# Performance work log

Measured on AMD Instinct MI355X. Metric: run time of the kernel, lower is better.

The kernel has to match this reference:

```python
import jax, jax.numpy as jnp
import numpy as np


def setup_inputs() -> dict:
    key = jax.random.key(0)
    kq, kk, kv = jax.random.split(key, 3)
    B, L, S, H, E = 2, 2048, 2048, 8, 64
    queries = jax.random.normal(kq, (B, L, H, E), dtype=jnp.float32)
    keys = jax.random.normal(kk, (B, S, H, E), dtype=jnp.float32)
    values = jax.random.normal(kv, (B, S, H, E), dtype=jnp.float32)
    a1 = jnp.float32(1.0)
    a2 = jnp.float32(1.0)
    return {"queries": queries, "keys": keys, "values": values, "a1": a1, "a2": a2}


def reference(queries, keys, values, a1, a2):
    # queries: (B,L,H,E); keys/values: (B,S,H,E)
    E = queries.shape[-1]
    scale = 1.0 / jnp.sqrt(jnp.float32(E))
    # shared QK scores: (B,H,L,S)
    qk = jnp.einsum('blhe,bshe->bhls', queries, keys) * scale
    # sparse branch: relu^2 (dropout = identity in eval)
    ssa = jnp.square(jax.nn.relu(qk))
    ssa_out = jnp.einsum('bhls,bshd->blhd', ssa, values)
    # dense branch: softmax over keys
    dsa = jax.nn.softmax(qk, axis=-1)
    dsa_out = jnp.einsum('bhls,bshd->blhd', dsa, values)
    w1 = jnp.exp(a1)
    w2 = jnp.exp(a2)
    alpha1 = w1 / (w1 + w2)
    alpha2 = w2 / (w1 + w2)
    return alpha1 * ssa_out + alpha2 * dsa_out
```

## Files before the change

### kernel.cpp

```cpp
#include <hip/hip_runtime.h>

typedef short short4v __attribute__((ext_vector_type(4)));
typedef short short8v __attribute__((ext_vector_type(8)));
typedef float float4v __attribute__((ext_vector_type(4)));
typedef unsigned short u16;

#define NB 2
#define NL 2048
#define NS 2048
#define NH 8
#define NE 64
#define HE (NH*NE)
#define NLT (NL/64)
#define NST (NS/64)
#define TILE_U16 4096

static __device__ __forceinline__ unsigned pk2bf(float a, float b) {
  union { float f; unsigned u; } x, y; x.f = a; y.f = b;
  return __builtin_amdgcn_perm(y.u + 0x8000u, x.u + 0x8000u, 0x07060302u);
}

#define GLD16(gp, lp) __builtin_amdgcn_global_load_lds( \
    (const __attribute__((address_space(1))) void*)(gp), \
    (__attribute__((address_space(3))) void*)(lp), 16, 0, 0)

static __device__ __forceinline__ int fK(int s) { return (s & 3) | ((s >> 1) & 4); }

__global__ __launch_bounds__(256)
void prepack(const float* __restrict__ kp, const float* __restrict__ vp,
             u16* __restrict__ kimg, u16* __restrict__ vimg)
{
  __shared__ __align__(16) u16 ldsv[TILE_U16];

  const int bid  = blockIdx.x;
  const int tile = bid >> 1;
  const int doV  = bid & 1;
  const int st = tile & (NST - 1);
  const int bh = tile >> 5;
  const int h  = bh & (NH - 1);
  const int b  = bh >> 3;
  const int s0 = st * 64;
  const size_t base = (size_t)b * NS * HE + h * NE;
  const int tid  = threadIdx.x;
  const int wv   = tid >> 6;
  const int lane = tid & 63;
  const int ln7  = lane & 7;

  if (!doV) {
    u16* kt = kimg + (size_t)tile * TILE_U16;
    for (int slot = tid; slot < 512; slot += 256) {
      const int srow = slot >> 3, p = slot & 7, c = p ^ fK(srow);
      const float* src = kp + base + (size_t)(s0 + srow) * HE + c * 8;
      float4 x0 = *(const float4*)src;
      float4 x1 = *(const float4*)(src + 4);
      unsigned d[4] = { pk2bf(x0.x, x0.y), pk2bf(x0.z, x0.w),
                        pk2bf(x1.x, x1.y), pk2bf(x1.z, x1.w) };
      *(int4*)(kt + slot * 8) = *(const int4*)d;
    }
    return;
  }

  u16* vt = vimg + (size_t)tile * TILE_U16;
  {
    const float* vcol = vp + base + (size_t)(s0 + wv * 16) * HE + lane;
    unsigned vr[8];
    #pragma unroll
    for (int jj = 0; jj < 8; ++jj)
      vr[jj] = pk2bf(vcol[(size_t)(2 * jj) * HE], vcol[(size_t)(2 * jj + 1) * HE]);
    #pragma unroll
    for (int i = 0; i < 2; ++i) {
      const int cs = (2 * wv + i) ^ ln7;
      int4 t4 = make_int4((int)vr[4*i+0], (int)vr[4*i+1],
                          (int)vr[4*i+2], (int)vr[4*i+3]);
      *(int4*)(&ldsv[lane * 64 + cs * 8]) = t4;
    }
  }
  __syncthreads();
  {
    const int4* s = (const int4*)ldsv;
    int4* dst = (int4*)vt;
    dst[tid]       = s[tid];
    dst[tid + 256] = s[tid + 256];
  }
}

__global__ __launch_bounds__(256, 2)
void assa_fwd(const float* __restrict__ qp, const u16* __restrict__ kimg,
              const u16* __restrict__ vimg, const float* __restrict__ a1p,
              const float* __restrict__ a2p, float* __restrict__ op)
{
  __shared__ __align__(16) u16 ldsb[4][2 * TILE_U16];

  const int tid  = threadIdx.x;
  const int wv   = tid >> 6;
  const int lane = tid & 63;
  const int ln15 = lane & 15;
  const int ln7  = lane & 7;
  const int quad = lane >> 4;

  const int bid = blockIdx.x;
  const int bh  = bid & 15;
  const int lt  = bid >> 4;
  const int h   = bh & (NH - 1);
  const int b   = bh >> 3;

  const int lbase = lt * 64 + wv * 16;

  short8v qf0, qf1;
  {
    const float* qrow = qp + ((size_t)(b * NL + lbase + ln15)) * HE + h * NE + quad * 8;
    float4 q0 = *(const float4*)(qrow);
    float4 q1 = *(const float4*)(qrow + 4);
    float4 q2 = *(const float4*)(qrow + 32);
    float4 q3 = *(const float4*)(qrow + 36);
    unsigned d0[4] = { pk2bf(0.125f*q0.x, 0.125f*q0.y), pk2bf(0.125f*q0.z, 0.125f*q0.w),
                       pk2bf(0.125f*q1.x, 0.125f*q1.y), pk2bf(0.125f*q1.z, 0.125f*q1.w) };
    unsigned d1[4] = { pk2bf(0.125f*q2.x, 0.125f*q2.y), pk2bf(0.125f*q2.z, 0.125f*q2.w),
                       pk2bf(0.125f*q3.x, 0.125f*q3.y), pk2bf(0.125f*q3.z, 0.125f*q3.w) };
    qf0 = *(const short8v*)d0;
    qf1 = *(const short8v*)d1;
  }

  short8v ones8;
  #pragma unroll
  for (int j = 0; j < 8; ++j) ones8[j] = (short)0x3F80;

  const size_t tbase = (size_t)bh * NST;

  float4v acc_s[4], acc_d[4], acc_l;
  #pragma unroll
  for (int t = 0; t < 4; ++t)
    #pragma unroll
    for (int r = 0; r < 4; ++r) { acc_s[t][r] = 0.0f; acc_d[t][r] = 0.0f; }
  #pragma unroll
  for (int r = 0; r < 4; ++r) acc_l[r] = 0.0f;

  auto dma_tile = [&](int st, int nb) {
    const int hf = wv & 1;
    const u16* g;
    u16* l;
    if (wv < 2) {
      g = kimg + (tbase + st) * TILE_U16 + hf * 2048 + lane * 8;
      l = &ldsb[nb][hf * 2048];
    } else {
      g = vimg + (tbase + st) * TILE_U16 + hf * 2048 + lane * 8;
      l = &ldsb[nb][TILE_U16 + hf * 2048];
    }
    GLD16(g,        l);
    GLD16(g +  512, l +  512);
    GLD16(g + 1024, l + 1024);
    GLD16(g + 1536, l + 1536);
  };

  dma_tile(0, 0);
  dma_tile(1, 1);
  dma_tile(2, 2);

  const int rperm = 8 * (ln15 >> 2) + (ln15 & 3);
  const int fk    = (ln15 & 3) | (((ln15 >> 2) & 1) << 2);

  for (int st = 0; st < NST; ++st) {
    if (st + 2 < NST)      asm volatile("s_waitcnt vmcnt(8)" ::: "memory");
    else if (st + 1 < NST) asm volatile("s_waitcnt vmcnt(4)" ::: "memory");
    else                   asm volatile("s_waitcnt vmcnt(0)" ::: "memory");
    __builtin_amdgcn_s_barrier();
    asm volatile("" ::: "memory");
    if (st + 3 < NST) dma_tile(st + 3, (st + 3) & 3);

    const u16* kb_l = ldsb[st & 3];
    const u16* vb_l = ldsb[st & 3] + TILE_U16;

    #pragma unroll
    for (int U = 0; U < 2; ++U) {
      float4v sa0, sa1;
      #pragma unroll
      for (int r = 0; r < 4; ++r) { sa0[r] = 0.0f; sa1[r] = 0.0f; }
      const u16* krow0 = &kb_l[(32 * U + rperm) * 64];
      const u16* krow1 = krow0 + 4 * 64;
      short8v kf00 = *(const short8v*)(krow0 + (quad ^ fk) * 8);
      short8v kf01 = *(const short8v*)(krow0 + ((4 + quad) ^ fk) * 8);
      short8v kf10 = *(const short8v*)(krow1 + (quad ^ fk) * 8);
      short8v kf11 = *(const short8v*)(krow1 + ((4 + quad) ^ fk) * 8);
      __builtin_amdgcn_s_setprio(1);
      sa0 = __builtin_amdgcn_mfma_f32_16x16x32_bf16(kf00, qf0, sa0, 0, 0, 0);
      sa0 = __builtin_amdgcn_mfma_f32_16x16x32_bf16(kf01, qf1, sa0, 0, 0, 0);
      sa1 = __builtin_amdgcn_mfma_f32_16x16x32_bf16(kf10, qf0, sa1, 0, 0, 0);
      sa1 = __builtin_amdgcn_mfma_f32_16x16x32_bf16(kf11, qf1, sa1, 0, 0, 0);
      __builtin_amdgcn_s_setprio(0);

      float ps[8], pd[8];
      #pragma unroll
      for (int r = 0; r < 4; ++r) {
        float s0 = sa0[r], s1 = sa1[r];
        float r0 = s0 > 0.0f ? s0 : 0.0f;
        float r1 = s1 > 0.0f ? s1 : 0.0f;
        ps[r] = r0 * r0;  ps[4 + r] = r1 * r1;
        pd[r] = __expf(s0); pd[4 + r] = __expf(s1);
      }
      unsigned da[4] = { pk2bf(ps[0], ps[1]), pk2bf(ps[2], ps[3]),
                         pk2bf(ps[4], ps[5]), pk2bf(ps[6], ps[7]) };
      unsigned db[4] = { pk2bf(pd[0], pd[1]), pk2bf(pd[2], pd[3]),
                         pk2bf(pd[4], pd[5]), pk2bf(pd[6], pd[7]) };
      short8v as8 = *(const short8v*)da;
      short8v ad8 = *(const short8v*)db;

      __builtin_amdgcn_s_setprio(1);
      acc_l = __builtin_amdgcn_mfma_f32_16x16x32_bf16(ad8, ones8, acc_l, 0, 0, 0);

      #pragma unroll
      for (int t = 0; t < 4; ++t) {
        short8v vf = *(const short8v*)(&vb_l[(t * 16 + ln15) * 64 +
                        (((4 * U + quad) ^ ln7) * 8)]);
        acc_s[t] = __builtin_amdgcn_mfma_f32_16x16x32_bf16(as8, vf, acc_s[t], 0, 0, 0);
        acc_d[t] = __builtin_amdgcn_mfma_f32_16x16x32_bf16(ad8, vf, acc_d[t], 0, 0, 0);
      }
      __builtin_amdgcn_s_setprio(0);
    }
  }

  const float w1 = __expf(a1p[0]), w2 = __expf(a2p[0]);
  const float al1 = w1 / (w1 + w2);
  const float al2 = w2 / (w1 + w2);

  float c_d[4];
  #pragma unroll
  for (int r = 0; r < 4; ++r) c_d[r] = al2 / acc_l[r];

  #pragma unroll
  for (int t = 0; t < 4; ++t) {
    #pragma unroll
    for (int r = 0; r < 4; ++r) {
      float val = al1 * acc_s[t][r] + c_d[r] * acc_d[t][r];
      const int l = lbase + quad * 4 + r;
      const int e = t * 16 + ln15;
      op[((size_t)(b * NL + l)) * HE + h * NE + e] = val;
    }
  }
}

extern "C" void kernel_launch(void* const* d_in, const int* in_sizes, int n_in,
                              void* d_out, int out_size, void* d_ws, size_t ws_size,
                              hipStream_t stream) {
  const float* q  = (const float*)d_in[0];
  const float* k  = (const float*)d_in[1];
  const float* v  = (const float*)d_in[2];
  const float* a1 = (const float*)d_in[3];
  const float* a2 = (const float*)d_in[4];
  float* out = (float*)d_out;
  (void)in_sizes; (void)n_in; (void)out_size; (void)ws_size;

  u16* kimg = (u16*)d_ws;
  u16* vimg = kimg + (size_t)NB * NH * NST * TILE_U16;

  prepack<<<dim3(NB * NH * NST * 2), dim3(256), 0, stream>>>(k, v, kimg, vimg);
  assa_fwd<<<dim3(NB * NH * NLT), dim3(256), 0, stream>>>(q, kimg, vimg, a1, a2, out);
}
```

Baseline: 114.3 us.

## Split key sequence across two wave groups per block with LDS reduction

Doubles the block to 512 threads so two groups of four waves each process alternating key tiles (split-K over S). Each group double-buffers its own K/V tiles, and the partial accumulators are merged through LDS at the end. It also folds log2(e) into the query scale so the softmax can use a raw v_exp_f32, rescaling the relu-squared branch by (ln2)^2 to compensate, and switches bf16 packing to the hardware v_cvt_pk_bf16_f32 instruction. The aim is more waves in flight across only 512 blocks. The costs are a shallower prefetch pipeline (vmcnt(0) every iteration), a final reduction pass, and fewer blocks per CU if registers are tight.

Measured after the change: 110.3 us. 1.04x faster.

```diff
diff --git a/kernel.cpp b/kernel.cpp
--- a/kernel.cpp
+++ b/kernel.cpp
@@ -18,6 +18,18 @@
 static __device__ __forceinline__ unsigned pk2bf(float a, float b) {
   union { float f; unsigned u; } x, y; x.f = a; y.f = b;
   return __builtin_amdgcn_perm(y.u + 0x8000u, x.u + 0x8000u, 0x07060302u);
+}
+
+static __device__ __forceinline__ unsigned cvtpk(float a, float b) {
+  unsigned r;
+  asm("v_cvt_pk_bf16_f32 %0, %1, %2" : "=v"(r) : "v"(a), "v"(b));
+  return r;
+}
+
+static __device__ __forceinline__ float fexp2(float x) {
+  float r;
+  asm("v_exp_f32 %0, %1" : "=v"(r) : "v"(x));
+  return r;
 }
 
 #define GLD16(gp, lp) __builtin_amdgcn_global_load_lds( \
@@ -84,15 +96,17 @@
   }
 }
 
-__global__ __launch_bounds__(256, 2)
+__global__ __launch_bounds__(512, 4)
 void assa_fwd(const float* __restrict__ qp, const u16* __restrict__ kimg,
               const u16* __restrict__ vimg, const float* __restrict__ a1p,
               const float* __restrict__ a2p, float* __restrict__ op)
 {
-  __shared__ __align__(16) u16 ldsb[4][2 * TILE_U16];
+  __shared__ __align__(16) u16 ldsb[2][2][2 * TILE_U16];
 
   const int tid  = threadIdx.x;
   const int wv   = tid >> 6;
+  const int ws   = wv & 3;
+  const int strm = wv >> 2;
   const int lane = tid & 63;
   const int ln15 = lane & 15;
   const int ln7  = lane & 7;
@@ -104,19 +118,20 @@
   const int h   = bh & (NH - 1);
   const int b   = bh >> 3;
 
-  const int lbase = lt * 64 + wv * 16;
+  const int lbase = lt * 64 + ws * 16;
 
   short8v qf0, qf1;
   {
+    const float qs = 0.125f * 1.44269504089f;
     const float* qrow = qp + ((size_t)(b * NL + lbase + ln15)) * HE + h * NE + quad * 8;
     float4 q0 = *(const float4*)(qrow);
     float4 q1 = *(const float4*)(qrow + 4);
     float4 q2 = *(const float4*)(qrow + 32);
     float4 q3 = *(const float4*)(qrow + 36);
-    unsigned d0[4] = { pk2bf(0.125f*q0.x, 0.125f*q0.y), pk2bf(0.125f*q0.z, 0.125f*q0.w),
-                       pk2bf(0.125f*q1.x, 0.125f*q1.y), pk2bf(0.125f*q1.z, 0.125f*q1.w) };
-    unsigned d1[4] = { pk2bf(0.125f*q2.x, 0.125f*q2.y), pk2bf(0.125f*q2.z, 0.125f*q2.w),
-                       pk2bf(0.125f*q3.x, 0.125f*q3.y), pk2bf(0.125f*q3.z, 0.125f*q3.w) };
+    unsigned d0[4] = { pk2bf(qs*q0.x, qs*q0.y), pk2bf(qs*q0.z, qs*q0.w),
+                       pk2bf(qs*q1.x, qs*q1.y), pk2bf(qs*q1.z, qs*q1.w) };
+    unsigned d1[4] = { pk2bf(qs*q2.x, qs*q2.y), pk2bf(qs*q2.z, qs*q2.w),
+                       pk2bf(qs*q3.x, qs*q3.y), pk2bf(qs*q3.z, qs*q3.w) };
     qf0 = *(const short8v*)d0;
     qf1 = *(const short8v*)d1;
   }
@@ -136,15 +151,15 @@
   for (int r = 0; r < 4; ++r) acc_l[r] = 0.0f;
 
   auto dma_tile = [&](int st, int nb) {
-    const int hf = wv & 1;
+    const int hf = ws & 1;
     const u16* g;
     u16* l;
-    if (wv < 2) {
+    if (ws < 2) {
       g = kimg + (tbase + st) * TILE_U16 + hf * 2048 + lane * 8;
-      l = &ldsb[nb][hf * 2048];
+      l = &ldsb[strm][nb][hf * 2048];
     } else {
       g = vimg + (tbase + st) * TILE_U16 + hf * 2048 + lane * 8;
-      l = &ldsb[nb][TILE_U16 + hf * 2048];
+      l = &ldsb[strm][nb][TILE_U16 + hf * 2048];
     }
     GLD16(g,        l);
     GLD16(g +  512, l +  512);
@@ -152,23 +167,19 @@
     GLD16(g + 1536, l + 1536);
   };
 
-  dma_tile(0, 0);
-  dma_tile(1, 1);
-  dma_tile(2, 2);
+  dma_tile(strm, 0);
 
   const int rperm = 8 * (ln15 >> 2) + (ln15 & 3);
   const int fk    = (ln15 & 3) | (((ln15 >> 2) & 1) << 2);
 
-  for (int st = 0; st < NST; ++st) {
-    if (st + 2 < NST)      asm volatile("s_waitcnt vmcnt(8)" ::: "memory");
-    else if (st + 1 < NST) asm volatile("s_waitcnt vmcnt(4)" ::: "memory");
-    else                   asm volatile("s_waitcnt vmcnt(0)" ::: "memory");
+  for (int it = 0; it < NST / 2; ++it) {
+    asm volatile("s_waitcnt vmcnt(0)" ::: "memory");
     __builtin_amdgcn_s_barrier();
     asm volatile("" ::: "memory");
-    if (st + 3 < NST) dma_tile(st + 3, (st + 3) & 3);
-
-    const u16* kb_l = ldsb[st & 3];
-    const u16* vb_l = ldsb[st & 3] + TILE_U16;
+    if (it + 1 < NST / 2) dma_tile(2 * (it + 1) + strm, (it + 1) & 1);
+
+    const u16* kb_l = ldsb[strm][it & 1];
+    const u16* vb_l = kb_l + TILE_U16;
 
     #pragma unroll
     for (int U = 0; U < 2; ++U) {
@@ -195,12 +206,12 @@
         float r0 = s0 > 0.0f ? s0 : 0.0f;
         float r1 = s1 > 0.0f ? s1 : 0.0f;
         ps[r] = r0 * r0;  ps[4 + r] = r1 * r1;
-        pd[r] = __expf(s0); pd[4 + r] = __expf(s1);
-      }
-      unsigned da[4] = { pk2bf(ps[0], ps[1]), pk2bf(ps[2], ps[3]),
-                         pk2bf(ps[4], ps[5]), pk2bf(ps[6], ps[7]) };
-      unsigned db[4] = { pk2bf(pd[0], pd[1]), pk2bf(pd[2], pd[3]),
-                         pk2bf(pd[4], pd[5]), pk2bf(pd[6], pd[7]) };
+        pd[r] = fexp2(s0); pd[4 + r] = fexp2(s1);
+      }
+      unsigned da[4] = { cvtpk(ps[0], ps[1]), cvtpk(ps[2], ps[3]),
+                         cvtpk(ps[4], ps[5]), cvtpk(ps[6], ps[7]) };
+      unsigned db[4] = { cvtpk(pd[0], pd[1]), cvtpk(pd[2], pd[3]),
+                         cvtpk(pd[4], pd[5]), cvtpk(pd[6], pd[7]) };
       short8v as8 = *(const short8v*)da;
       short8v ad8 = *(const short8v*)db;
 
@@ -218,22 +229,51 @@
     }
   }
 
-  const float w1 = __expf(a1p[0]), w2 = __expf(a2p[0]);
-  const float al1 = w1 / (w1 + w2);
-  const float al2 = w2 / (w1 + w2);
-
-  float c_d[4];
-  #pragma unroll
-  for (int r = 0; r < 4; ++r) c_d[r] = al2 / acc_l[r];
-
-  #pragma unroll
-  for (int t = 0; t < 4; ++t) {
-    #pragma unroll
-    for (int r = 0; r < 4; ++r) {
-      float val = al1 * acc_s[t][r] + c_d[r] * acc_d[t][r];
-      const int l = lbase + quad * 4 + r;
-      const int e = t * 16 + ln15;
-      op[((size_t)(b * NL + l)) * HE + h * NE + e] = val;
+  __syncthreads();
+  float* red = (float*)&ldsb[0][0][0];
+  const int idx = ws * 64 + lane;
+  if (strm == 1) {
+    #pragma unroll
+    for (int t = 0; t < 4; ++t)
+      #pragma unroll
+      for (int r = 0; r < 4; ++r) {
+        red[(t * 4 + r) * 256 + idx]        = acc_s[t][r];
+        red[(16 + t * 4 + r) * 256 + idx]   = acc_d[t][r];
+      }
+    #pragma unroll
+    for (int r = 0; r < 4; ++r)
+      red[(32 + r) * 256 + idx] = acc_l[r];
+  }
+  __syncthreads();
+  if (strm == 0) {
+    #pragma unroll
+    for (int t = 0; t < 4; ++t)
+      #pragma unroll
+      for (int r = 0; r < 4; ++r) {
+        acc_s[t][r] += red[(t * 4 + r) * 256 + idx];
+        acc_d[t][r] += red[(16 + t * 4 + r) * 256 + idx];
+      }
+    #pragma unroll
+    for (int r = 0; r < 4; ++r)
+      acc_l[r] += red[(32 + r) * 256 + idx];
+
+    const float w1 = __expf(a1p[0]), w2 = __expf(a2p[0]);
+    const float al1 = (w1 / (w1 + w2)) * 0.48045301391820142f;
+    const float al2 = w2 / (w1 + w2);
+
+    float c_d[4];
+    #pragma unroll
+    for (int r = 0; r < 4; ++r) c_d[r] = al2 / acc_l[r];
+
+    #pragma unroll
+    for (int t = 0; t < 4; ++t) {
+      #pragma unroll
+      for (int r = 0; r < 4; ++r) {
+        float val = al1 * acc_s[t][r] + c_d[r] * acc_d[t][r];
+        const int l = lbase + quad * 4 + r;
+        const int e = t * 16 + ln15;
+        op[((size_t)(b * NL + l)) * HE + h * NE + e] = val;
+      }
     }
   }
 }
@@ -253,5 +293,5 @@
   u16* vimg = kimg + (size_t)NB * NH * NST * TILE_U16;
 
   prepack<<<dim3(NB * NH * NST * 2), dim3(256), 0, stream>>>(k, v, kimg, vimg);
-  assa_fwd<<<dim3(NB * NH * NLT), dim3(256), 0, stream>>>(q, kimg, vimg, a1, a2, out);
-}
+  assa_fwd<<<dim3(NB * NH * NLT), dim3(512), 0, stream>>>(q, kimg, vimg, a1, a2, out);
+}
```
